# Optimization experiments

Measured on AMD Instinct MI355X. Metric: run time of the kernel, lower is better.

Reference implementation:

```python
import jax, jax.numpy as jnp
import numpy as np

TRUNC = (24, 24, 24)
OUT = (32, 32, 32)


def setup_inputs() -> dict:
    key = jax.random.key(0)
    x = jax.random.normal(key, (8, 32, 48, 48, 48), dtype=jnp.float32)
    return {"x": x}


def reference(x):
    # "DCT" as implemented in the source: real part of an ortho-normalized 3D FFT
    x_dct = jnp.real(jnp.fft.fftn(x, axes=(2, 3, 4), norm='ortho'))
    # crop to low-frequency corner, zero-pad up to output_size
    x_crop = x_dct[:, :, :TRUNC[0], :TRUNC[1], :TRUNC[2]]
    pad = ((0, 0), (0, 0),
           (0, OUT[0] - TRUNC[0]),
           (0, OUT[1] - TRUNC[1]),
           (0, OUT[2] - TRUNC[2]))
    x_pad = jnp.pad(x_crop, pad)
    # inverse transform on the output_size grid, keep real part
    x_idct = jnp.real(jnp.fft.ifftn(x_pad, axes=(2, 3, 4), norm='ortho'))
    return x_idct
```

## Files before the change

kernel.cpp:

```cpp
#include <hip/hip_runtime.h>
#include <math.h>


#define TWO_PI_48 0.13089969389957470f
#define TWO_PI_32 0.19634954084936207f
#define NORM_F    1.6611664e-05f

typedef _Float16 half8  __attribute__((ext_vector_type(8)));
typedef _Float16 half4v __attribute__((ext_vector_type(4)));
typedef float    f32x4  __attribute__((ext_vector_type(4)));

__device__ _Float16 T1frag[2][3][2][64][8];
__device__ _Float16 T2frag[2][3][2][64][8];
__device__ __align__(16) _Float16 TK2frag[2][4][3][64][8];
__device__ __align__(16) _Float16 MB2frag[2][4][2][64][8];
__device__ __align__(16) _Float16 TB3frag[2][2][2][64][8];

__device__ int g_twdone = 0;

__global__ void k_init_tw() {
  if (g_twdone) return;
  const int idx = blockIdx.x * 256 + threadIdx.x;
  if (idx < 3072) {
    const int j  = idx & 7;
    const int l  = (idx >> 3) & 63;
    const int ks = (idx >> 9) & 1;
    const int t  = idx >> 10;
    const int k  = ks * 32 + (l >> 4) * 8 + j;
    {
      const int m = t * 16 + (l & 15);
      float v = 0.f;
      if (k < 48) {
        const float a = (float)(((m % 24) * k) % 48) * TWO_PI_48;
        v = (m < 24) ? cosf(a) : -sinf(a);
      }
      const _Float16 h = (_Float16)v;
      T1frag[0][t][ks][l][j] = h;
      T1frag[1][t][ks][l][j] = (_Float16)(v - (float)h);
    }
    {
      const int c = t * 16 + (l & 15);
      float v = 0.f;
      if (k < 48) {
        const float a = (float)(((c % 24) * k) % 48) * TWO_PI_48;
        v = (c < 24) ? cosf(a) : sinf(a);
      }
      const _Float16 h = (_Float16)v;
      T2frag[0][t][ks][l][j] = h;
      T2frag[1][t][ks][l][j] = (_Float16)(v - (float)h);
    }
  } else if (idx < 3072 + 6144) {
    const int local = idx - 3072;
    const int j = local & 7, l = (local >> 3) & 63;
    const int rest = local >> 9;
    const int ks = rest % 3, mt = rest / 3;
    const int m   = mt * 16 + (l & 15);
    const int kap = ks * 32 + (l >> 4) * 8 + j;
    const int n1  = kap % 48;
    const bool isVi = kap >= 48;
    const int m1  = m & 31;
    const bool isWi = m >= 32;
    float acc = 0.f;
    for (int k1 = 0; k1 < 24; ++k1) {
      float s32v, c32v, s48v, c48v;
      sincosf((float)((k1 * m1) % 32) * TWO_PI_32, &s32v, &c32v);
      sincosf((float)((k1 * n1) % 48) * TWO_PI_48, &s48v, &c48v);
      acc = fmaf(isWi ? s32v : c32v, isVi ? s48v : c48v, acc);
    }
    const _Float16 h = (_Float16)acc;
    TK2frag[0][mt][ks][l][j] = h;
    TK2frag[1][mt][ks][l][j] = (_Float16)(acc - (float)h);
  } else if (idx < 3072 + 6144 + 4096) {
    const int local = idx - (3072 + 6144);
    const int j = local & 7, l = (local >> 3) & 63;
    const int rest = local >> 9;
    const int ks = rest & 1, mt = rest >> 1;
    const int m   = mt * 16 + (l & 15);
    const int kap = ks * 32 + (l >> 4) * 8 + j;
    float v = 0.f;
    if (kap < 48) {
      const int k2 = kap % 24;
      const int m2 = m & 31;
      float s, c;
      sincosf((float)((k2 * m2) % 32) * TWO_PI_32, &s, &c);
      if (m < 32) v = (kap < 24) ? c : -s;
      else        v = (kap < 24) ? s :  c;
    }
    const _Float16 h = (_Float16)v;
    MB2frag[0][mt][ks][l][j] = h;
    MB2frag[1][mt][ks][l][j] = (_Float16)(v - (float)h);
  } else if (idx < 15360) {
    const int local = idx - (3072 + 6144 + 4096);
    const int j = local & 7, l = (local >> 3) & 63;
    const int rest = local >> 9;
    const int ks = rest & 1, nt = rest >> 1;
    const int m3  = nt * 16 + (l & 15);
    const int kap = ks * 32 + (l >> 4) * 8 + j;
    float v = 0.f;
    if (kap < 48) {
      const int k3 = kap % 24;
      float s, c;
      sincosf((float)((k3 * m3) % 32) * TWO_PI_32, &s, &c);
      v = (kap < 24) ? c : -s;
    }
    const _Float16 h = (_Float16)v;
    TB3frag[0][nt][ks][l][j] = h;
    TB3frag[1][nt][ks][l][j] = (_Float16)(v - (float)h);
  }
}

__device__ inline void split8(const float* qf, half8& h, half8& lo) {
#pragma unroll
  for (int j = 0; j < 8; ++j) {
    const _Float16 hh = (_Float16)qf[j];
    h[j]  = hh;
    lo[j] = (_Float16)(qf[j] - (float)hh);
  }
}

__global__ __launch_bounds__(256, 3) void k1_waveslab(const float* __restrict__ x,
                                                      float2* __restrict__ V) {
  const int bx   = blockIdx.x;
  const int bc   = blockIdx.y;
  const int wv   = threadIdx.x >> 6;
  const int lane = threadIdx.x & 63;
  const int n1   = bx * 4 + wv;

  __shared__ __align__(16) float pool[4 * 48 * 68];
  float* U  = pool + wv * (48 * 68);
  float* D2 = U;

  const int c16  = lane & 15;
  const int kgrp = lane >> 4;
  const int kb   = kgrp * 8;

  half8 t1h[3][2], t1l[3][2], t2h[3][2], t2l[3][2];
#pragma unroll
  for (int mt = 0; mt < 3; ++mt)
#pragma unroll
    for (int ks = 0; ks < 2; ++ks) {
      t1h[mt][ks] = *(const half8*)&T1frag[0][mt][ks][lane][0];
      t1l[mt][ks] = *(const half8*)&T1frag[1][mt][ks][lane][0];
      t2h[mt][ks] = *(const half8*)&T2frag[0][mt][ks][lane][0];
      t2l[mt][ks] = *(const half8*)&T2frag[1][mt][ks][lane][0];
    }

#pragma unroll
  for (int p = 0; p < 3; ++p) {
    const int fl = lane + 64 * p;
    const int row = fl >> 2, c4 = fl & 3;
    *(f32x4*)&U[row * 68 + 48 + c4 * 4] = (f32x4){};
  }

  const float* xs = x + (size_t)(bc * 48 + n1) * 2304;

  float4 fa0, fb0, fa1, fb1;
  {
    const float4* p0 = (const float4*)(xs + c16 * 48 + kb);
    fa0 = p0[0]; fb0 = p0[1];
    const int k1i = 32 + kb;
    if (k1i < 48) {
      const float4* p1 = (const float4*)(xs + c16 * 48 + k1i);
      fa1 = p1[0]; fb1 = p1[1];
    } else { fa1 = make_float4(0.f,0.f,0.f,0.f); fb1 = fa1; }
  }

#pragma unroll
  for (int nt = 0; nt < 3; ++nt) {
    float4 na0, nb0, na1, nb1;
    if (nt < 2) {
      const int c = (nt + 1) * 16 + c16;
      const float4* p0 = (const float4*)(xs + c * 48 + kb);
      na0 = p0[0]; nb0 = p0[1];
      const int k1i = 32 + kb;
      if (k1i < 48) {
        const float4* p1 = (const float4*)(xs + c * 48 + k1i);
        na1 = p1[0]; nb1 = p1[1];
      } else { na1 = make_float4(0.f,0.f,0.f,0.f); nb1 = na1; }
    }

    f32x4 acc0 = {}, acc1 = {}, acc2 = {};
#pragma unroll
    for (int ks = 0; ks < 2; ++ks) {
      const float4 qa = ks ? fa1 : fa0;
      const float4 qb = ks ? fb1 : fb0;
      const float qf[8] = {qa.x, qa.y, qa.z, qa.w, qb.x, qb.y, qb.z, qb.w};
      half8 bh, bl;
      split8(qf, bh, bl);
#pragma unroll
      for (int mt = 0; mt < 3; ++mt) {
        f32x4& acc = (mt == 0) ? acc0 : (mt == 1) ? acc1 : acc2;
        acc = __builtin_amdgcn_mfma_f32_16x16x32_f16(t1h[mt][ks], bh, acc, 0, 0, 0);
        acc = __builtin_amdgcn_mfma_f32_16x16x32_f16(t1h[mt][ks], bl, acc, 0, 0, 0);
        acc = __builtin_amdgcn_mfma_f32_16x16x32_f16(t1l[mt][ks], bh, acc, 0, 0, 0);
      }
    }

    {
      const int cc = nt * 16 + c16;
#pragma unroll
      for (int mt = 0; mt < 3; ++mt) {
        const int r0 = mt * 16 + kgrp * 4;
        const f32x4 acc = (mt == 0) ? acc0 : (mt == 1) ? acc1 : acc2;
#pragma unroll
        for (int r = 0; r < 4; ++r)
          U[(r0 + r) * 68 + cc] = acc[r];
      }
    }

    fa0 = na0; fb0 = nb0; fa1 = na1; fb1 = nb1;
  }

  f32x4 a2[3][3] = {};
#pragma unroll
  for (int ks = 0; ks < 2; ++ks) {
#pragma unroll
    for (int mt = 0; mt < 3; ++mt) {
      const float4 q0 = *(const float4*)&U[(mt * 16 + c16) * 68 + ks * 32 + kb];
      const float4 q1 = *(const float4*)&U[(mt * 16 + c16) * 68 + ks * 32 + kb + 4];
      const float qf[8] = {q0.x, q0.y, q0.z, q0.w, q1.x, q1.y, q1.z, q1.w};
      half8 ah, al;
      split8(qf, ah, al);
#pragma unroll
      for (int nt2 = 0; nt2 < 3; ++nt2) {
        a2[mt][nt2] = __builtin_amdgcn_mfma_f32_16x16x32_f16(ah, t2h[nt2][ks], a2[mt][nt2], 0, 0, 0);
        a2[mt][nt2] = __builtin_amdgcn_mfma_f32_16x16x32_f16(ah, t2l[nt2][ks], a2[mt][nt2], 0, 0, 0);
        a2[mt][nt2] = __builtin_amdgcn_mfma_f32_16x16x32_f16(al, t2h[nt2][ks], a2[mt][nt2], 0, 0, 0);
      }
    }
  }

#pragma unroll
  for (int mt = 0; mt < 3; ++mt)
#pragma unroll
    for (int nt2 = 0; nt2 < 3; ++nt2) {
      const int r0 = mt * 16 + kgrp * 4;
      const int cc = nt2 * 16 + c16;
#pragma unroll
      for (int r = 0; r < 4; ++r)
        D2[(r0 + r) * 68 + cc] = a2[mt][nt2][r];
    }

#pragma unroll
  for (int q = 0; q < 9; ++q) {
    const int idx = lane + 64 * q;
    const int k3 = idx / 24, k2 = idx % 24;
    const float grr = D2[k3 * 68 + k2];
    const float gis = D2[(k3 + 24) * 68 + k2 + 24];
    const float gir = D2[(k3 + 24) * 68 + k2];
    const float grs = D2[k3 * 68 + k2 + 24];
    V[(size_t)bc * 27648 + (size_t)k3 * 1152 + n1 * 24 + k2] =
        make_float2(grr + gis, gir - grs);
  }
}

__global__ __launch_bounds__(192) void k2_mfma(const float2* __restrict__ V,
                                               float2* __restrict__ W) {
  const int k3   = blockIdx.x;
  const int byy  = blockIdx.y;
  const int tid  = threadIdx.x;
  const int lane = tid & 63;
  const int w    = tid >> 6;

  __shared__ __align__(16) float Bb[48 * 100];

  half8 kth[4][3], ktl[4][3];
#pragma unroll
  for (int mt = 0; mt < 4; ++mt)
#pragma unroll
    for (int ks = 0; ks < 3; ++ks) {
      kth[mt][ks] = *(const half8*)&TK2frag[0][mt][ks][lane][0];
      ktl[mt][ks] = *(const half8*)&TK2frag[1][mt][ks][lane][0];
    }

  const int kbase = (lane >> 4) * 8;
  const int c16   = lane & 15;
  const int cc    = w * 16 + c16;
  const int sE    = cc / 24, k2E = cc % 24;
  const int rbase = (lane >> 4) * 4;

  float4 vr[6];
  {
    const float4* g0 = (const float4*)(V + ((size_t)((byy * 4 + 0) * 24 + k3)) * 1152);
    const float4* g1 = (const float4*)(V + ((size_t)((byy * 4 + 1) * 24 + k3)) * 1152);
#pragma unroll
    for (int jj = 0; jj < 6; ++jj)
      vr[jj] = (jj < 3 ? g0 : g1)[tid + 192 * (jj % 3)];
  }

  for (int g = 0; g < 2; ++g) {
    const int bcp = byy * 2 + g;

    if (g) __syncthreads();

#pragma unroll
    for (int jj = 0; jj < 6; ++jj) {
      const int s = jj / 3;
      const int r = tid + 192 * (jj % 3);
      const int n1 = r / 12, c4 = r % 12;
      const float4 f = vr[jj];
      float* bp = &Bb[(s * 24 + c4 * 2) * 100 + n1];
      bp[0]   = f.x;  bp[48]  = f.y;
      bp[100] = f.z;  bp[148] = f.w;
    }
    if (g < 1) {
      const float4* g0 = (const float4*)(V + ((size_t)((bcp * 2 + 2) * 24 + k3)) * 1152);
      const float4* g1 = (const float4*)(V + ((size_t)((bcp * 2 + 3) * 24 + k3)) * 1152);
#pragma unroll
      for (int jj = 0; jj < 6; ++jj)
        vr[jj] = (jj < 3 ? g0 : g1)[tid + 192 * (jj % 3)];
    }
    __syncthreads();

    f32x4 a0 = {}, a1 = {}, a2 = {}, a3 = {};
#pragma unroll
    for (int ks = 0; ks < 3; ++ks) {
      const float4 q0 = *(const float4*)&Bb[cc * 100 + ks * 32 + kbase];
      const float4 q1 = *(const float4*)&Bb[cc * 100 + ks * 32 + kbase + 4];
      const float qf[8] = {q0.x, q0.y, q0.z, q0.w, q1.x, q1.y, q1.z, q1.w};
      half8 bh, bl;
      split8(qf, bh, bl);
#pragma unroll
      for (int mt = 0; mt < 4; ++mt) {
        f32x4& acc = (mt == 0) ? a0 : (mt == 1) ? a1 : (mt == 2) ? a2 : a3;
        acc = __builtin_amdgcn_mfma_f32_16x16x32_f16(kth[mt][ks], bh, acc, 0, 0, 0);
        acc = __builtin_amdgcn_mfma_f32_16x16x32_f16(kth[mt][ks], bl, acc, 0, 0, 0);
        acc = __builtin_amdgcn_mfma_f32_16x16x32_f16(ktl[mt][ks], bh, acc, 0, 0, 0);
      }
    }

    const int bc = bcp * 2 + sE;
    float2* wp = W + (size_t)bc * 18432 + (size_t)k3 * 24 + k2E;
#pragma unroll
    for (int mt = 0; mt < 2; ++mt) {
      const f32x4 wr = (mt == 0) ? a0 : a1;
      const f32x4 wi = (mt == 0) ? a2 : a3;
#pragma unroll
      for (int r = 0; r < 4; ++r) {
        const int m1 = mt * 16 + rbase + r;
        wp[(size_t)m1 * 576] = make_float2(wr[r], wi[r]);
      }
    }
  }
}

__global__ __launch_bounds__(128) void k3_mfma(const float2* __restrict__ W,
                                               float* __restrict__ out) {
  const int m1   = blockIdx.x;
  const int byy  = blockIdx.y;
  const int tid  = threadIdx.x;
  const int lane = tid & 63;
  const int w    = tid >> 6;

  __shared__ __align__(16) float Bt[32 * 68];
  __shared__ __align__(16) float Zb[32 * 68];

  half8 mbh[4][2], mbl[4][2];
#pragma unroll
  for (int mt = 0; mt < 4; ++mt)
#pragma unroll
    for (int ks = 0; ks < 2; ++ks) {
      mbh[mt][ks] = *(const half8*)&MB2frag[0][mt][ks][lane][0];
      mbl[mt][ks] = *(const half8*)&MB2frag[1][mt][ks][lane][0];
    }
  half8 tb3h[2], tb3l[2];
#pragma unroll
  for (int ks = 0; ks < 2; ++ks) {
    tb3h[ks] = *(const half8*)&TB3frag[0][w][ks][lane][0];
    tb3l[ks] = *(const half8*)&TB3frag[1][w][ks][lane][0];
  }

  for (int i = tid; i < 8 * 68; i += 128)  Bt[(24 + i / 68) * 68 + (i % 68)] = 0.f;
  for (int i = tid; i < 24 * 20; i += 128) Bt[(i / 20) * 68 + 48 + (i % 20)] = 0.f;
  for (int i = tid; i < 32 * 20; i += 128) Zb[(i / 20) * 68 + 48 + (i % 20)] = 0.f;

  const int kbase = (lane >> 4) * 8;
  const int c16   = lane & 15;
  const int cc    = w * 16 + c16;
  const int rbase = (lane >> 4) * 4;

  float4 vr0, vr1, vr2;
  {
    const float4* g4 = (const float4*)(W + (size_t)(byy * 2) * 18432 + (size_t)m1 * 576);
    vr0 = g4[tid];
    vr1 = g4[tid + 128];
    if (tid < 32) vr2 = g4[tid + 256];
  }

  for (int g = 0; g < 2; ++g) {
    const int bc = byy * 2 + g;

    {
      const float4 fr[3] = {vr0, vr1, vr2};
#pragma unroll
      for (int jj = 0; jj < 3; ++jj) {
        const int i4 = tid + 128 * jj;
        if (jj < 2 || tid < 32) {
          const int k3 = i4 / 12, c4 = i4 % 12;
          const float4 f = fr[jj];
          Bt[k3 * 68 + 2 * c4]          = f.x;
          Bt[k3 * 68 + 24 + 2 * c4]     = f.y;
          Bt[k3 * 68 + 2 * c4 + 1]      = f.z;
          Bt[k3 * 68 + 24 + 2 * c4 + 1] = f.w;
        }
      }
    }
    if (g < 1) {
      const float4* g4 = (const float4*)(W + (size_t)(bc + 1) * 18432 + (size_t)m1 * 576);
      vr0 = g4[tid];
      vr1 = g4[tid + 128];
      if (tid < 32) vr2 = g4[tid + 256];
    }
    __syncthreads();

    f32x4 z0 = {}, z1 = {}, z2 = {}, z3 = {};
#pragma unroll
    for (int ks = 0; ks < 2; ++ks) {
      const float4 q0 = *(const float4*)&Bt[cc * 68 + ks * 32 + kbase];
      const float4 q1 = *(const float4*)&Bt[cc * 68 + ks * 32 + kbase + 4];
      const float qf[8] = {q0.x, q0.y, q0.z, q0.w, q1.x, q1.y, q1.z, q1.w};
      half8 bh, bl;
      split8(qf, bh, bl);
#pragma unroll
      for (int mt = 0; mt < 4; ++mt) {
        f32x4& acc = (mt == 0) ? z0 : (mt == 1) ? z1 : (mt == 2) ? z2 : z3;
        acc = __builtin_amdgcn_mfma_f32_16x16x32_f16(mbh[mt][ks], bh, acc, 0, 0, 0);
        acc = __builtin_amdgcn_mfma_f32_16x16x32_f16(mbh[mt][ks], bl, acc, 0, 0, 0);
        acc = __builtin_amdgcn_mfma_f32_16x16x32_f16(mbl[mt][ks], bh, acc, 0, 0, 0);
      }
    }
    if (cc < 24) {
#pragma unroll
      for (int mt = 0; mt < 4; ++mt) {
        const f32x4 acc = (mt == 0) ? z0 : (mt == 1) ? z1 : (mt == 2) ? z2 : z3;
        const int row0 = mt * 16 + rbase;
#pragma unroll
        for (int r = 0; r < 4; ++r) {
          const int row = row0 + r;
          if (row < 32) Zb[row * 68 + cc]              = acc[r];
          else          Zb[(row - 32) * 68 + 24 + cc]  = acc[r];
        }
      }
    }
    __syncthreads();

    f32x4 o0 = {}, o1 = {};
#pragma unroll
    for (int ks = 0; ks < 2; ++ks) {
#pragma unroll
      for (int mt = 0; mt < 2; ++mt) {
        const float4 q0 = *(const float4*)&Zb[(mt * 16 + c16) * 68 + ks * 32 + kbase];
        const float4 q1 = *(const float4*)&Zb[(mt * 16 + c16) * 68 + ks * 32 + kbase + 4];
        const float qf[8] = {q0.x, q0.y, q0.z, q0.w, q1.x, q1.y, q1.z, q1.w};
        half8 ah, al;
        split8(qf, ah, al);
        f32x4& acc = (mt == 0) ? o0 : o1;
        acc = __builtin_amdgcn_mfma_f32_16x16x32_f16(ah, tb3h[ks], acc, 0, 0, 0);
        acc = __builtin_amdgcn_mfma_f32_16x16x32_f16(ah, tb3l[ks], acc, 0, 0, 0);
        acc = __builtin_amdgcn_mfma_f32_16x16x32_f16(al, tb3h[ks], acc, 0, 0, 0);
      }
    }
    float* op = out + (size_t)(bc * 32 + m1) * 1024;
#pragma unroll
    for (int mt = 0; mt < 2; ++mt) {
      const f32x4 acc = (mt == 0) ? o0 : o1;
#pragma unroll
      for (int r = 0; r < 4; ++r) {
        const int m2 = mt * 16 + rbase + r;
        op[m2 * 32 + cc] = acc[r] * NORM_F;
      }
    }
  }

  if (tid == 0 && blockIdx.x == 0 && blockIdx.y == 0) g_twdone = 1;
}

extern "C" void kernel_launch(void* const* d_in, const int* in_sizes, int n_in,
                              void* d_out, int out_size, void* d_ws, size_t ws_size,
                              hipStream_t stream) {
  const float* x = (const float*)d_in[0];
  float* out = (float*)d_out;
  float2* V = (float2*)d_ws;
  float2* W = (float2*)((char*)d_ws + 56623104);

  k_init_tw   <<<dim3(60), dim3(256), 0, stream>>>();
  k1_waveslab <<<dim3(12, 256), dim3(256), 0, stream>>>(x, V);
  k2_mfma     <<<dim3(24, 64), dim3(192), 0, stream>>>(V, W);
  k3_mfma     <<<dim3(32, 128), dim3(128), 0, stream>>>(W, out);
}
```

Measured before the change: 78.17 us.

## Process two n1 slabs per wave in k1, halving block threads

The first-stage kernel now runs two waves per block, with each wave handling two n1 slabs instead of one. All global loads for both slabs are issued upfront, and the T1/T2 twiddle fragments are loaded once and reused across both slabs. T2 fragments are deferred until after the first GEMM to limit register pressure. This aims to expose more memory-level parallelism and amortize the twiddle loads, at the cost of more registers per wave and fewer waves resident per CU, since shared memory per block is unchanged.

```diff
diff --git a/kernel.cpp b/kernel.cpp
--- a/kernel.cpp
+++ b/kernel.cpp
@@ -118,72 +118,33 @@
   }
 }
 
-__global__ __launch_bounds__(256, 3) void k1_waveslab(const float* __restrict__ x,
-                                                      float2* __restrict__ V) {
-  const int bx   = blockIdx.x;
-  const int bc   = blockIdx.y;
-  const int wv   = threadIdx.x >> 6;
-  const int lane = threadIdx.x & 63;
-  const int n1   = bx * 4 + wv;
-
-  __shared__ __align__(16) float pool[4 * 48 * 68];
-  float* U  = pool + wv * (48 * 68);
-  float* D2 = U;
-
-  const int c16  = lane & 15;
-  const int kgrp = lane >> 4;
-  const int kb   = kgrp * 8;
-
-  half8 t1h[3][2], t1l[3][2], t2h[3][2], t2l[3][2];
-#pragma unroll
-  for (int mt = 0; mt < 3; ++mt)
+__device__ inline void load_xf(const float* xs, int c16, int kb, float4 f[3][2][2]) {
+  const int k1i = 32 + kb;
+#pragma unroll
+  for (int nt = 0; nt < 3; ++nt) {
+    const int c = nt * 16 + c16;
+    const float4* p0 = (const float4*)(xs + c * 48 + kb);
+    f[nt][0][0] = p0[0]; f[nt][0][1] = p0[1];
+    if (k1i < 48) {
+      const float4* p1 = (const float4*)(xs + c * 48 + k1i);
+      f[nt][1][0] = p1[0]; f[nt][1][1] = p1[1];
+    } else {
+      f[nt][1][0] = make_float4(0.f, 0.f, 0.f, 0.f);
+      f[nt][1][1] = make_float4(0.f, 0.f, 0.f, 0.f);
+    }
+  }
+}
+
+__device__ inline void gemm1_dump(const float4 xf[3][2][2],
+                                  const half8 t1h[3][2], const half8 t1l[3][2],
+                                  float* U, int c16, int kgrp) {
+#pragma unroll
+  for (int nt = 0; nt < 3; ++nt) {
+    f32x4 acc0 = {}, acc1 = {}, acc2 = {};
 #pragma unroll
     for (int ks = 0; ks < 2; ++ks) {
-      t1h[mt][ks] = *(const half8*)&T1frag[0][mt][ks][lane][0];
-      t1l[mt][ks] = *(const half8*)&T1frag[1][mt][ks][lane][0];
-      t2h[mt][ks] = *(const half8*)&T2frag[0][mt][ks][lane][0];
-      t2l[mt][ks] = *(const half8*)&T2frag[1][mt][ks][lane][0];
-    }
-
-#pragma unroll
-  for (int p = 0; p < 3; ++p) {
-    const int fl = lane + 64 * p;
-    const int row = fl >> 2, c4 = fl & 3;
-    *(f32x4*)&U[row * 68 + 48 + c4 * 4] = (f32x4){};
-  }
-
-  const float* xs = x + (size_t)(bc * 48 + n1) * 2304;
-
-  float4 fa0, fb0, fa1, fb1;
-  {
-    const float4* p0 = (const float4*)(xs + c16 * 48 + kb);
-    fa0 = p0[0]; fb0 = p0[1];
-    const int k1i = 32 + kb;
-    if (k1i < 48) {
-      const float4* p1 = (const float4*)(xs + c16 * 48 + k1i);
-      fa1 = p1[0]; fb1 = p1[1];
-    } else { fa1 = make_float4(0.f,0.f,0.f,0.f); fb1 = fa1; }
-  }
-
-#pragma unroll
-  for (int nt = 0; nt < 3; ++nt) {
-    float4 na0, nb0, na1, nb1;
-    if (nt < 2) {
-      const int c = (nt + 1) * 16 + c16;
-      const float4* p0 = (const float4*)(xs + c * 48 + kb);
-      na0 = p0[0]; nb0 = p0[1];
-      const int k1i = 32 + kb;
-      if (k1i < 48) {
-        const float4* p1 = (const float4*)(xs + c * 48 + k1i);
-        na1 = p1[0]; nb1 = p1[1];
-      } else { na1 = make_float4(0.f,0.f,0.f,0.f); nb1 = na1; }
-    }
-
-    f32x4 acc0 = {}, acc1 = {}, acc2 = {};
-#pragma unroll
-    for (int ks = 0; ks < 2; ++ks) {
-      const float4 qa = ks ? fa1 : fa0;
-      const float4 qb = ks ? fb1 : fb0;
+      const float4 qa = xf[nt][ks][0];
+      const float4 qb = xf[nt][ks][1];
       const float qf[8] = {qa.x, qa.y, qa.z, qa.w, qb.x, qb.y, qb.z, qb.w};
       half8 bh, bl;
       split8(qf, bh, bl);
@@ -195,22 +156,22 @@
         acc = __builtin_amdgcn_mfma_f32_16x16x32_f16(t1l[mt][ks], bh, acc, 0, 0, 0);
       }
     }
-
-    {
-      const int cc = nt * 16 + c16;
-#pragma unroll
-      for (int mt = 0; mt < 3; ++mt) {
-        const int r0 = mt * 16 + kgrp * 4;
-        const f32x4 acc = (mt == 0) ? acc0 : (mt == 1) ? acc1 : acc2;
-#pragma unroll
-        for (int r = 0; r < 4; ++r)
-          U[(r0 + r) * 68 + cc] = acc[r];
-      }
-    }
-
-    fa0 = na0; fb0 = nb0; fa1 = na1; fb1 = nb1;
-  }
-
+    const int cc = nt * 16 + c16;
+#pragma unroll
+    for (int mt = 0; mt < 3; ++mt) {
+      const int r0 = mt * 16 + kgrp * 4;
+      const f32x4 acc = (mt == 0) ? acc0 : (mt == 1) ? acc1 : acc2;
+#pragma unroll
+      for (int r = 0; r < 4; ++r)
+        U[(r0 + r) * 68 + cc] = acc[r];
+    }
+  }
+}
+
+__device__ inline void gemm2_epi(float* U, const half8 t2h[3][2], const half8 t2l[3][2],
+                                 float2* __restrict__ V, int bc, int n1,
+                                 int c16, int kgrp, int kb, int lane) {
+  float* D2 = U;
   f32x4 a2[3][3] = {};
 #pragma unroll
   for (int ks = 0; ks < 2; ++ks) {
@@ -229,7 +190,6 @@
       }
     }
   }
-
 #pragma unroll
   for (int mt = 0; mt < 3; ++mt)
 #pragma unroll
@@ -240,7 +200,6 @@
       for (int r = 0; r < 4; ++r)
         D2[(r0 + r) * 68 + cc] = a2[mt][nt2][r];
     }
-
 #pragma unroll
   for (int q = 0; q < 9; ++q) {
     const int idx = lane + 64 * q;
@@ -252,6 +211,62 @@
     V[(size_t)bc * 27648 + (size_t)k3 * 1152 + n1 * 24 + k2] =
         make_float2(grr + gis, gir - grs);
   }
+}
+
+__global__ __launch_bounds__(128, 3) void k1_waveslab(const float* __restrict__ x,
+                                                      float2* __restrict__ V) {
+  const int bx   = blockIdx.x;
+  const int bc   = blockIdx.y;
+  const int wv   = threadIdx.x >> 6;
+  const int lane = threadIdx.x & 63;
+  const int n1A  = bx * 4 + wv * 2;
+  const int n1B  = n1A + 1;
+
+  __shared__ __align__(16) float pool[4 * 48 * 68];
+  float* UA = pool + (wv * 2 + 0) * (48 * 68);
+  float* UB = pool + (wv * 2 + 1) * (48 * 68);
+
+  const int c16  = lane & 15;
+  const int kgrp = lane >> 4;
+  const int kb   = kgrp * 8;
+
+  const float* xc = x + (size_t)(bc * 48) * 2304;
+
+  float4 xfA[3][2][2], xfB[3][2][2];
+  load_xf(xc + (size_t)n1A * 2304, c16, kb, xfA);
+  load_xf(xc + (size_t)n1B * 2304, c16, kb, xfB);
+
+  half8 t1h[3][2], t1l[3][2];
+#pragma unroll
+  for (int mt = 0; mt < 3; ++mt)
+#pragma unroll
+    for (int ks = 0; ks < 2; ++ks) {
+      t1h[mt][ks] = *(const half8*)&T1frag[0][mt][ks][lane][0];
+      t1l[mt][ks] = *(const half8*)&T1frag[1][mt][ks][lane][0];
+    }
+
+#pragma unroll
+  for (int p = 0; p < 3; ++p) {
+    const int fl = lane + 64 * p;
+    const int row = fl >> 2, c4 = fl & 3;
+    *(f32x4*)&UA[row * 68 + 48 + c4 * 4] = (f32x4){};
+    *(f32x4*)&UB[row * 68 + 48 + c4 * 4] = (f32x4){};
+  }
+
+  gemm1_dump(xfA, t1h, t1l, UA, c16, kgrp);
+  gemm1_dump(xfB, t1h, t1l, UB, c16, kgrp);
+
+  half8 t2h[3][2], t2l[3][2];
+#pragma unroll
+  for (int mt = 0; mt < 3; ++mt)
+#pragma unroll
+    for (int ks = 0; ks < 2; ++ks) {
+      t2h[mt][ks] = *(const half8*)&T2frag[0][mt][ks][lane][0];
+      t2l[mt][ks] = *(const half8*)&T2frag[1][mt][ks][lane][0];
+    }
+
+  gemm2_epi(UA, t2h, t2l, V, bc, n1A, c16, kgrp, kb, lane);
+  gemm2_epi(UB, t2h, t2l, V, bc, n1B, c16, kgrp, kb, lane);
 }
 
 __global__ __launch_bounds__(192) void k2_mfma(const float2* __restrict__ V,
@@ -484,7 +499,7 @@
   float2* W = (float2*)((char*)d_ws + 56623104);
 
   k_init_tw   <<<dim3(60), dim3(256), 0, stream>>>();
-  k1_waveslab <<<dim3(12, 256), dim3(256), 0, stream>>>(x, V);
+  k1_waveslab <<<dim3(12, 256), dim3(128), 0, stream>>>(x, V);
   k2_mfma     <<<dim3(24, 64), dim3(192), 0, stream>>>(V, W);
   k3_mfma     <<<dim3(32, 128), dim3(128), 0, stream>>>(W, out);
 }
```

Result: slower. 86.03 us (+10.1%).
